# Kernel tuning notes

Hardware: AMD Instinct MI355X
Metric: run time of the kernel (lower is better)

The kernel has to match this reference:

```python
import jax, jax.numpy as jnp
import numpy as np

EMB = 1024
HID = 2048
HEADS = 16
CONV = 4


def causal_conv1d(z, w):
    # z: [B, H, T], w: [H, K] depthwise causal conv
    K = w.shape[1]
    T = z.shape[-1]
    zp = jnp.pad(z, ((0, 0), (0, 0), (K - 1, 0)))  # [B, H, T+K-1]
    out = jnp.zeros_like(z)
    for k in range(K):  # tiny fixed loop over taps (K<=4)
        out = out + w[None, :, k, None] * jax.lax.dynamic_slice_in_dim(zp, k, T, axis=2)
    return out


def linear_scan(a, b):
    # h_t = a_t * h_{t-1} + b_t along last axis; associative scan
    def combine(c1, c2):
        a1, b1 = c1
        a2, b2 = c2
        return a1 * a2, a2 * b1 + b2
    _, h = jax.lax.associative_scan(combine, (a, b), axis=-1)
    return h


def setup_inputs() -> dict:
    key = jax.random.key(0)
    k1, k2, k3, k4 = jax.random.split(key, 4)
    x = jax.random.normal(k1, (4, 2048, EMB), dtype=jnp.float32)
    w1 = jax.random.normal(k2, (3 * HID, EMB), dtype=jnp.float32) * (EMB ** -0.5)
    w2 = jax.random.normal(k3, (EMB, HID), dtype=jnp.float32) * (HID ** -0.5)
    conv_weight = jax.random.normal(k4, (HID, CONV), dtype=jnp.float32) * (CONV ** -0.5)
    return {"x": x, "w1": w1, "w2": w2, "conv_weight": conv_weight}


def reference(x, w1, w2, conv_weight):
    bsz, seq_len, _ = x.shape
    head_dim = HID // HEADS
    y = jnp.einsum("bse,he->bsh", x, w1)  # [B, S, 3*HID]
    out1, z, h = jnp.split(y, 3, axis=-1)
    z = jnp.swapaxes(z, 1, 2)  # [B, HID, S]
    h = jnp.swapaxes(h, 1, 2)
    z = causal_conv1d(z, conv_weight)
    z = jax.nn.sigmoid(z)
    z = z.reshape(bsz * HEADS, head_dim, seq_len)
    h = h.reshape(bsz * HEADS, head_dim, seq_len)
    h = linear_scan(1.0 - z, z * h)
    out2 = jnp.swapaxes(h.reshape(bsz, HID, seq_len), 1, 2)  # [B, S, HID]
    out = jax.nn.silu(out1) * out2
    return jnp.einsum("bsh,eh->bse", out, w2)
```

## Files before the change

### kernel.cpp

```cpp
#include <hip/hip_runtime.h>
#include <cstdint>

#define EMB 1024
#define HID 2048
#define BATCH 4
#define SEQ 2048
#define MROWS (BATCH * SEQ)
#define N1 (3 * HID)
#define K1 EMB
#define N2 EMB
#define K2 HID

#define NX (MROWS * EMB)
#define NW1 (N1 * K1)
#define NW2 (N2 * K2)

#define SEG 32
#define SLEN (SEQ / SEG)

typedef unsigned short ushort_t;
typedef __bf16 bf16x8 __attribute__((ext_vector_type(8)));
typedef float f32x4 __attribute__((ext_vector_type(4)));
typedef ushort_t us4 __attribute__((ext_vector_type(4)));

__device__ __forceinline__ ushort_t f2bf(float f) {
    uint32_t u = __builtin_bit_cast(uint32_t, f);
    u += 0x7fffu + ((u >> 16) & 1u);
    return (ushort_t)(u >> 16);
}
__device__ __forceinline__ float bf2f(ushort_t h) {
    uint32_t u = ((uint32_t)h) << 16;
    return __builtin_bit_cast(float, u);
}
__device__ __forceinline__ float bflo(uint32_t v) {
    return __builtin_bit_cast(float, v << 16);
}
__device__ __forceinline__ float bfhi(uint32_t v) {
    return __builtin_bit_cast(float, v & 0xffff0000u);
}
__device__ __forceinline__ float sigm(float x) {
    return 1.f / (1.f + __expf(-x));
}

__device__ __forceinline__ void gload_lds16(const ushort_t* g, const ushort_t* l) {
    __builtin_amdgcn_global_load_lds(
        (const __attribute__((address_space(1))) void*)(uintptr_t)(g),
        (__attribute__((address_space(3))) void*)(uint32_t)(uintptr_t)(l),
        16, 0, 0);
}

__global__ __launch_bounds__(256) void cvt_kernel(
    const float* __restrict__ x, const float* __restrict__ w1,
    const float* __restrict__ w2, ushort_t* __restrict__ xb,
    ushort_t* __restrict__ w1b, ushort_t* __restrict__ w2b) {
    const int i = (blockIdx.x * 256 + threadIdx.x) * 4;
    const float* s;
    ushort_t* d;
    if (i < NX) {
        s = x + i; d = xb + i;
    } else if (i < NX + NW1) {
        s = w1 + (i - NX); d = w1b + (i - NX);
    } else {
        s = w2 + (i - NX - NW1); d = w2b + (i - NX - NW1);
    }
    const float4 v = *(const float4*)s;
    us4 o;
    o.x = f2bf(v.x); o.y = f2bf(v.y); o.z = f2bf(v.z); o.w = f2bf(v.w);
    *(us4*)d = o;
}

template <bool OUT_BF16>
__global__ __launch_bounds__(256) void gemm_bt(
    const ushort_t* __restrict__ A, const ushort_t* __restrict__ B,
    void* __restrict__ Cv, int M, int N, int K) {
    __shared__ ushort_t sA[2 * 128 * 32];
    __shared__ ushort_t sB[2 * 128 * 32];

    const int tid  = threadIdx.x;
    const int lane = tid & 63;
    const int wave = tid >> 6;
    const int quad = lane >> 4;
    const int l16  = lane & 15;
    const long tm0 = (long)blockIdx.y * 128;
    const long tn0 = (long)blockIdx.x * 128;
    const int wm = (wave & 1) * 64;
    const int wn = (wave >> 1) * 64;

    f32x4 acc[4][4] = {};

    const int ar0 = tid >> 2;
    const int ar1 = (tid + 256) >> 2;
    const int kq  = (tid & 3) ^ ((ar0 >> 1) & 3);
    const int ac  = kq * 8;
    const ushort_t* gA = A + (size_t)tm0 * K;
    const ushort_t* gB = B + (size_t)tn0 * K;

    const int rsw = (l16 >> 1) & 3;
    const int aoff = (quad ^ rsw) * 8 + l16 * 32;

    for (int k0 = 0; k0 < K; k0 += 64) {
        __syncthreads();
#pragma unroll
        for (int p = 0; p < 2; ++p) {
            const int kp = k0 + p * 32;
            ushort_t* pA = &sA[p * 4096];
            ushort_t* pB = &sB[p * 4096];
            gload_lds16(gA + (size_t)ar0 * K + kp + ac, pA + wave * 512);
            gload_lds16(gA + (size_t)ar1 * K + kp + ac, pA + 2048 + wave * 512);
            gload_lds16(gB + (size_t)ar0 * K + kp + ac, pB + wave * 512);
            gload_lds16(gB + (size_t)ar1 * K + kp + ac, pB + 2048 + wave * 512);
        }
        __syncthreads();

#pragma unroll
        for (int p = 0; p < 2; ++p) {
            const ushort_t* pA = &sA[p * 4096];
            const ushort_t* pB = &sB[p * 4096];
            bf16x8 af[4], bfr[4];
#pragma unroll
            for (int i = 0; i < 4; ++i)
                af[i] = *(const bf16x8*)&pA[(wm + i * 16) * 32 + aoff];
#pragma unroll
            for (int j = 0; j < 4; ++j)
                bfr[j] = *(const bf16x8*)&pB[(wn + j * 16) * 32 + aoff];
#pragma unroll
            for (int i = 0; i < 4; ++i)
#pragma unroll
                for (int j = 0; j < 4; ++j)
                    acc[i][j] = __builtin_amdgcn_mfma_f32_16x16x32_bf16(
                        af[i], bfr[j], acc[i][j], 0, 0, 0);
        }
    }

#pragma unroll
    for (int i = 0; i < 4; ++i) {
        const long row0 = tm0 + wm + i * 16 + quad * 4;
#pragma unroll
        for (int j = 0; j < 4; ++j) {
            const long col = tn0 + wn + j * 16 + l16;
#pragma unroll
            for (int r = 0; r < 4; ++r) {
                if constexpr (OUT_BF16) {
                    ((ushort_t*)Cv)[(size_t)(row0 + r) * N + col] = f2bf(acc[i][j][r]);
                } else {
                    ((float*)Cv)[(size_t)(row0 + r) * N + col] = acc[i][j][r];
                }
            }
        }
    }
}

__device__ __forceinline__ void lda4(bf16x8 (&af)[2][4], const ushort_t* c,
                                     int arow, int quad, int sw) {
#pragma unroll
    for (int s = 0; s < 2; ++s)
#pragma unroll
        for (int i = 0; i < 4; ++i)
            af[s][i] = *(const bf16x8*)&c[(arow + i * 16) * 64 +
                                          (((s * 4 + quad) ^ sw) << 3)];
}
__device__ __forceinline__ void ldb2(bf16x8 (&bfr)[2][2], const ushort_t* c,
                                     int bcol, int quad, int sw) {
#pragma unroll
    for (int s = 0; s < 2; ++s)
#pragma unroll
        for (int j = 0; j < 2; ++j)
            bfr[s][j] = *(const bf16x8*)&c[(bcol + j * 16) * 64 +
                                           (((s * 4 + quad) ^ sw) << 3)];
}
template <int QM, int QN>
__device__ __forceinline__ void mm16(f32x4 (&acc)[8][4],
                                     const bf16x8 (&af)[2][4],
                                     const bf16x8 (&bfr)[2][2]) {
#pragma unroll
    for (int s = 0; s < 2; ++s)
#pragma unroll
        for (int i = 0; i < 4; ++i)
#pragma unroll
            for (int j = 0; j < 2; ++j)
                acc[QM * 4 + i][QN * 2 + j] =
                    __builtin_amdgcn_mfma_f32_16x16x32_bf16(
                        af[s][i], bfr[s][j], acc[QM * 4 + i][QN * 2 + j], 0, 0, 0);
}

template <bool OUT_BF16>
__global__ __launch_bounds__(512, 2) void gemm256(
    const ushort_t* __restrict__ A, const ushort_t* __restrict__ B,
    void* __restrict__ Cv, int M, int N, int K) {
    __shared__ __align__(16) ushort_t sA[2][2][8192];
    __shared__ __align__(16) ushort_t sB[2][2][8192];

    const int tid  = threadIdx.x;
    const int lane = tid & 63;
    const int wave = tid >> 6;
    const int wm   = wave >> 2;
    const int wn   = wave & 3;
    const int quad = lane >> 4;
    const int l15  = lane & 15;
    const int sw   = lane & 7;

    int wg = blockIdx.x;
    const int nwg = gridDim.x;
    if ((nwg & 7) == 0) wg = (wg & 7) * (nwg >> 3) + (wg >> 3);
    const int nbx = N >> 8;
    const int bx = wg % nbx;
    const int by = wg / nbx;
    const long tm0 = (long)by << 8;
    const long tn0 = (long)bx << 8;

    const ushort_t* gA = A + (size_t)tm0 * K;
    const ushort_t* gB = B + (size_t)tn0 * K;

    const int l8 = lane >> 3;
    const int ss = (lane & 7) ^ l8;
    const uint32_t rA = (uint32_t)((wave & 3) * 16 + l8 + (wave >> 2) * 128);
    const int cB = wave * 16 + l8;
    const uint32_t rB = (uint32_t)((cB >> 5) * 64 + (cB & 31));
    const uint32_t offA0 = rA * (uint32_t)K + (uint32_t)ss * 8u;
    const uint32_t offA1 = offA0 + 8u * (uint32_t)K;
    const uint32_t offB0 = rB * (uint32_t)K + (uint32_t)ss * 8u;
    const uint32_t offB1 = offB0 + 8u * (uint32_t)K;

    const auto stA = [&](int tt, int q) {
        ushort_t* d = &sA[tt & 1][q][wave << 10];
        const size_t ko = (size_t)tt * 64 + (size_t)q * 64 * (size_t)K;
        gload_lds16(gA + ko + offA0, d);
        gload_lds16(gA + ko + offA1, d + 512);
    };
    const auto stB = [&](int tt, int q) {
        ushort_t* d = &sB[tt & 1][q][wave << 10];
        const size_t ko = (size_t)tt * 64 + (size_t)q * 32 * (size_t)K;
        gload_lds16(gB + ko + offB0, d);
        gload_lds16(gB + ko + offB1, d + 512);
    };

    const int arow = wm * 64 + l15;
    const int bcol = wn * 32 + l15;

    f32x4 acc[8][4] = {};
    bf16x8 af0[2][4], af1[2][4], bf0[2][2], bf1[2][2];

    const int NT = K >> 6;

    stA(0, 0); stB(0, 0); stB(0, 1); stA(0, 1);
    asm volatile("s_waitcnt vmcnt(0)" ::: "memory");
    __builtin_amdgcn_s_barrier();

    for (int T = 0; T < NT; ++T) {
        const int cur = T & 1;
        const ushort_t* a0 = &sA[cur][0][0];
        const ushort_t* a1 = &sA[cur][1][0];
        const ushort_t* b0 = &sB[cur][0][0];
        const ushort_t* b1 = &sB[cur][1][0];
        const bool st1 = (T + 1 < NT);

        lda4(af0, a0, arow, quad, sw);
        ldb2(bf0, b0, bcol, quad, sw);
        ldb2(bf1, b1, bcol, quad, sw);
        lda4(af1, a1, arow, quad, sw);
        if (st1) {
            stA(T + 1, 0); stB(T + 1, 0);
            stB(T + 1, 1); stA(T + 1, 1);
        }
        __builtin_amdgcn_s_setprio(1);
        mm16<0, 0>(acc, af0, bf0);
        mm16<0, 1>(acc, af0, bf1);
        mm16<1, 0>(acc, af1, bf0);
        mm16<1, 1>(acc, af1, bf1);
        __builtin_amdgcn_s_setprio(0);
        if (st1) asm volatile("s_waitcnt vmcnt(0)" ::: "memory");
        __builtin_amdgcn_s_barrier();
    }

#pragma unroll
    for (int ai = 0; ai < 8; ++ai) {
        const long row0 = tm0 + wm * 128 + (ai >> 2) * 64 + (ai & 3) * 16 + quad * 4;
#pragma unroll
        for (int bj = 0; bj < 4; ++bj) {
            const long col = tn0 + wn * 64 + (bj >> 1) * 32 + (bj & 1) * 16 + l15;
#pragma unroll
            for (int r = 0; r < 4; ++r) {
                if constexpr (OUT_BF16) {
                    ((ushort_t*)Cv)[(size_t)(row0 + r) * N + col] = f2bf(acc[ai][bj][r]);
                } else {
                    ((float*)Cv)[(size_t)(row0 + r) * N + col] = acc[ai][bj][r];
                }
            }
        }
    }
}

__global__ __launch_bounds__(256) void scan_part1(
    const ushort_t* __restrict__ y, const float* __restrict__ cw,
    float* __restrict__ Ag, float* __restrict__ Bg) {
    const int gid = blockIdx.x * 256 + threadIdx.x;
    const int ch  = (gid & 1023) * 2;
    const int bs  = gid >> 10;
    const int b   = bs >> 5;
    const int seg = bs & 31;
    const int t0  = seg * SLEN;
    const size_t rowbase = (size_t)b * SEQ;
    const ushort_t* yz = y + 2048 + ch;
    const ushort_t* yh = y + 4096 + ch;

    float w[2][4];
#pragma unroll
    for (int c = 0; c < 2; ++c)
#pragma unroll
        for (int k = 0; k < 4; ++k) w[c][k] = cw[(ch + c) * 4 + k];

    auto ld2 = [&](const ushort_t* p, int t) -> uint32_t {
        return *(const uint32_t*)(p + (rowbase + (size_t)t) * 6144);
    };
    auto zpair = [&](int t, float* out) {
        if (t < 0) { out[0] = 0.f; out[1] = 0.f; }
        else { uint32_t v = ld2(yz, t); out[0] = bflo(v); out[1] = bfhi(v); }
    };

    float z1[2], z2[2], z3[2], A[2] = {1.f, 1.f}, Bv[2] = {0.f, 0.f};
    zpair(t0 - 1, z1); zpair(t0 - 2, z2); zpair(t0 - 3, z3);

#pragma unroll 4
    for (int t = t0; t < t0 + SLEN; ++t) {
        const uint32_t vz = ld2(yz, t);
        const uint32_t vh = ld2(yh, t);
        const float zr[2] = {bflo(vz), bfhi(vz)};
        const float hr[2] = {bflo(vh), bfhi(vh)};
#pragma unroll
        for (int c = 0; c < 2; ++c) {
            const float cv = w[c][0] * z3[c] + w[c][1] * z2[c] +
                             w[c][2] * z1[c] + w[c][3] * zr[c];
            const float s = sigm(cv);
            z3[c] = z2[c]; z2[c] = z1[c]; z1[c] = zr[c];
            const float a = 1.f - s;
            A[c] *= a;
            Bv[c] = a * Bv[c] + s * hr[c];
        }
    }
    const size_t idx = ((size_t)b * SEG + seg) * HID + ch;
    *(float2*)&Ag[idx] = make_float2(A[0], A[1]);
    *(float2*)&Bg[idx] = make_float2(Bv[0], Bv[1]);
}

__global__ __launch_bounds__(256) void scan_part2(
    const float* __restrict__ Ag, const float* __restrict__ Bg,
    float* __restrict__ Cr) {
    const int gid = blockIdx.x * 256 + threadIdx.x;
    const int b  = gid >> 11;
    const int ch = gid & 2047;
    float carry = 0.f;
#pragma unroll
    for (int s = 0; s < SEG; ++s) {
        const size_t idx = ((size_t)b * SEG + s) * HID + ch;
        Cr[idx] = carry;
        carry = Ag[idx] * carry + Bg[idx];
    }
}

__global__ __launch_bounds__(256) void scan_part3(
    const ushort_t* __restrict__ y, const float* __restrict__ cw,
    const float* __restrict__ Cr, ushort_t* __restrict__ u) {
    const int gid = blockIdx.x * 256 + threadIdx.x;
    const int ch  = (gid & 1023) * 2;
    const int bs  = gid >> 10;
    const int b   = bs >> 5;
    const int seg = bs & 31;
    const int t0  = seg * SLEN;
    const size_t rowbase = (size_t)b * SEQ;
    const ushort_t* yo = y + ch;
    const ushort_t* yz = y + 2048 + ch;
    const ushort_t* yh = y + 4096 + ch;

    float w[2][4];
#pragma unroll
    for (int c = 0; c < 2; ++c)
#pragma unroll
        for (int k = 0; k < 4; ++k) w[c][k] = cw[(ch + c) * 4 + k];

    auto ld2 = [&](const ushort_t* p, int t) -> uint32_t {
        return *(const uint32_t*)(p + (rowbase + (size_t)t) * 6144);
    };
    auto zpair = [&](int t, float* out) {
        if (t < 0) { out[0] = 0.f; out[1] = 0.f; }
        else { uint32_t v = ld2(yz, t); out[0] = bflo(v); out[1] = bfhi(v); }
    };

    const size_t cidx = ((size_t)b * SEG + seg) * HID + ch;
    float h[2] = {Cr[cidx], Cr[cidx + 1]};
    float z1[2], z2[2], z3[2];
    zpair(t0 - 1, z1); zpair(t0 - 2, z2); zpair(t0 - 3, z3);

#pragma unroll 4
    for (int t = t0; t < t0 + SLEN; ++t) {
        const uint32_t vz = ld2(yz, t);
        const uint32_t vh = ld2(yh, t);
        const uint32_t vo = ld2(yo, t);
        const float zr[2] = {bflo(vz), bfhi(vz)};
        const float hr[2] = {bflo(vh), bfhi(vh)};
        const float o1[2] = {bflo(vo), bfhi(vo)};
        ushort_t res[2];
#pragma unroll
        for (int c = 0; c < 2; ++c) {
            const float cv = w[c][0] * z3[c] + w[c][1] * z2[c] +
                             w[c][2] * z1[c] + w[c][3] * zr[c];
            const float s = sigm(cv);
            z3[c] = z2[c]; z2[c] = z1[c]; z1[c] = zr[c];
            h[c] = (1.f - s) * h[c] + s * hr[c];
            const float sil = o1[c] * sigm(o1[c]);
            res[c] = f2bf(sil * h[c]);
        }
        *(uint32_t*)&u[(rowbase + (size_t)t) * (size_t)HID + ch] =
            (uint32_t)res[0] | ((uint32_t)res[1] << 16);
    }
}

extern "C" void kernel_launch(void* const* d_in, const int* in_sizes, int n_in,
                              void* d_out, int out_size, void* d_ws, size_t ws_size,
                              hipStream_t stream) {
    const float* x  = (const float*)d_in[0];
    const float* w1 = (const float*)d_in[1];
    const float* w2 = (const float*)d_in[2];
    const float* cw = (const float*)d_in[3];
    char* ws = (char*)d_ws;

    ushort_t* xb  = (ushort_t*)(ws);
    ushort_t* w1b = (ushort_t*)(ws + (size_t)16777216);
    ushort_t* w2b = (ushort_t*)(ws + (size_t)29360128);
    ushort_t* y   = (ushort_t*)(ws + (size_t)33554432);
    ushort_t* u   = (ushort_t*)(ws + (size_t)134217728);
    float* Ag = (float*)(ws);
    float* Bg = (float*)(ws + (size_t)1048576);
    float* Cr = (float*)(ws + (size_t)2097152);
    float* out = (float*)d_out;

    cvt_kernel<<<16384, 256, 0, stream>>>(x, w1, w2, xb, w1b, w2b);
    gemm256<true><<<dim3(768), 512, 0, stream>>>(xb, w1b, (void*)y, MROWS, N1, K1);
    scan_part1<<<512, 256, 0, stream>>>(y, cw, Ag, Bg);
    scan_part2<<<32, 256, 0, stream>>>(Ag, Bg, Cr);
    scan_part3<<<512, 256, 0, stream>>>(y, cw, Cr, u);
    gemm_bt<false><<<dim3(N2 / 128, MROWS / 128), 256, 0, stream>>>(
        u, w2b, (void*)out, MROWS, N2, K2);
}
```

Measured before the change: 306.0 us.

## Split-K second GEMM with atomics and vectorize first GEMM epilogue stores

The second GEMM becomes a split-K kernel with two K halves. Each half accumulates into a zeroed fp32 output through relaxed atomic adds, which doubles the block count from 512 to 1024. Separately, the first GEMM swaps MFMA operands so the accumulator layout is transposed, letting each lane write 4 contiguous outputs as one packed bf16 uint2 store instead of scalar strided stores. Costs are an extra memset of the output and atomic traffic for every output element.

```diff
diff --git a/kernel.cpp b/kernel.cpp
--- a/kernel.cpp
+++ b/kernel.cpp
@@ -69,10 +69,9 @@
     *(us4*)d = o;
 }
 
-template <bool OUT_BF16>
-__global__ __launch_bounds__(256) void gemm_bt(
+__global__ __launch_bounds__(256) void gemm_bt_ks(
     const ushort_t* __restrict__ A, const ushort_t* __restrict__ B,
-    void* __restrict__ Cv, int M, int N, int K) {
+    float* __restrict__ C, int M, int N, int K, int KLEN) {
     __shared__ ushort_t sA[2 * 128 * 32];
     __shared__ ushort_t sB[2 * 128 * 32];
 
@@ -92,13 +91,14 @@
     const int ar1 = (tid + 256) >> 2;
     const int kq  = (tid & 3) ^ ((ar0 >> 1) & 3);
     const int ac  = kq * 8;
-    const ushort_t* gA = A + (size_t)tm0 * K;
-    const ushort_t* gB = B + (size_t)tn0 * K;
+    const size_t kofs = (size_t)blockIdx.z * (size_t)KLEN;
+    const ushort_t* gA = A + (size_t)tm0 * K + kofs;
+    const ushort_t* gB = B + (size_t)tn0 * K + kofs;
 
     const int rsw = (l16 >> 1) & 3;
     const int aoff = (quad ^ rsw) * 8 + l16 * 32;
 
-    for (int k0 = 0; k0 < K; k0 += 64) {
+    for (int k0 = 0; k0 < KLEN; k0 += 64) {
         __syncthreads();
 #pragma unroll
         for (int p = 0; p < 2; ++p) {
@@ -140,11 +140,9 @@
             const long col = tn0 + wn + j * 16 + l16;
 #pragma unroll
             for (int r = 0; r < 4; ++r) {
-                if constexpr (OUT_BF16) {
-                    ((ushort_t*)Cv)[(size_t)(row0 + r) * N + col] = f2bf(acc[i][j][r]);
-                } else {
-                    ((float*)Cv)[(size_t)(row0 + r) * N + col] = acc[i][j][r];
-                }
+                __hip_atomic_fetch_add(&C[(size_t)(row0 + r) * N + col],
+                                       acc[i][j][r], __ATOMIC_RELAXED,
+                                       __HIP_MEMORY_SCOPE_AGENT);
             }
         }
     }
@@ -180,7 +178,7 @@
             for (int j = 0; j < 2; ++j)
                 acc[QM * 4 + i][QN * 2 + j] =
                     __builtin_amdgcn_mfma_f32_16x16x32_bf16(
-                        af[s][i], bfr[s][j], acc[QM * 4 + i][QN * 2 + j], 0, 0, 0);
+                        bfr[s][j], af[s][i], acc[QM * 4 + i][QN * 2 + j], 0, 0, 0);
 }
 
 template <bool OUT_BF16>
@@ -274,17 +272,21 @@
 
 #pragma unroll
     for (int ai = 0; ai < 8; ++ai) {
-        const long row0 = tm0 + wm * 128 + (ai >> 2) * 64 + (ai & 3) * 16 + quad * 4;
+        const long m = tm0 + wm * 128 + (ai >> 2) * 64 + (ai & 3) * 16 + l15;
 #pragma unroll
         for (int bj = 0; bj < 4; ++bj) {
-            const long col = tn0 + wn * 64 + (bj >> 1) * 32 + (bj & 1) * 16 + l15;
-#pragma unroll
-            for (int r = 0; r < 4; ++r) {
-                if constexpr (OUT_BF16) {
-                    ((ushort_t*)Cv)[(size_t)(row0 + r) * N + col] = f2bf(acc[ai][bj][r]);
-                } else {
-                    ((float*)Cv)[(size_t)(row0 + r) * N + col] = acc[ai][bj][r];
-                }
+            const long n0 = tn0 + wn * 64 + (bj >> 1) * 32 + (bj & 1) * 16 + quad * 4;
+            if constexpr (OUT_BF16) {
+                const uint32_t lo = (uint32_t)f2bf(acc[ai][bj][0]) |
+                                    ((uint32_t)f2bf(acc[ai][bj][1]) << 16);
+                const uint32_t hi = (uint32_t)f2bf(acc[ai][bj][2]) |
+                                    ((uint32_t)f2bf(acc[ai][bj][3]) << 16);
+                *(uint2*)&((ushort_t*)Cv)[(size_t)m * N + n0] = make_uint2(lo, hi);
+            } else {
+                float4 v;
+                v.x = acc[ai][bj][0]; v.y = acc[ai][bj][1];
+                v.z = acc[ai][bj][2]; v.w = acc[ai][bj][3];
+                *(float4*)&((float*)Cv)[(size_t)m * N + n0] = v;
             }
         }
     }
@@ -438,6 +440,7 @@
     scan_part1<<<512, 256, 0, stream>>>(y, cw, Ag, Bg);
     scan_part2<<<32, 256, 0, stream>>>(Ag, Bg, Cr);
     scan_part3<<<512, 256, 0, stream>>>(y, cw, Cr, u);
-    gemm_bt<false><<<dim3(N2 / 128, MROWS / 128), 256, 0, stream>>>(
-        u, w2b, (void*)out, MROWS, N2, K2);
-}
+    hipMemsetAsync(d_out, 0, (size_t)MROWS * N2 * 4, stream);
+    gemm_bt_ks<<<dim3(N2 / 128, MROWS / 128, 2), 256, 0, stream>>>(
+        u, w2b, out, MROWS, N2, K2, K2 / 2);
+}
```

Result: slower. 357.5 us (+16.8%).

## Replace second GEMM with double-buffered 256x128 tile kernel

Applied to the files above, without the earlier changes.

Swaps the simple 128x128 gemm_bt used for the output projection for a new gemm_mn kernel. It uses 512 threads, 256x128 tiles, a double-buffered LDS pipeline that prefetches the next K-tile while MFMAs run, s_setprio around the MFMA block, and an XCD-aware remapping of workgroup IDs. The intent is to hide global-load latency and improve data reuse per block. In exchange it uses more LDS per block and launches only 256 workgroups, which may reduce occupancy and balance across CUs.

```diff
diff --git a/kernel.cpp b/kernel.cpp
--- a/kernel.cpp
+++ b/kernel.cpp
@@ -67,87 +67,6 @@
     us4 o;
     o.x = f2bf(v.x); o.y = f2bf(v.y); o.z = f2bf(v.z); o.w = f2bf(v.w);
     *(us4*)d = o;
-}
-
-template <bool OUT_BF16>
-__global__ __launch_bounds__(256) void gemm_bt(
-    const ushort_t* __restrict__ A, const ushort_t* __restrict__ B,
-    void* __restrict__ Cv, int M, int N, int K) {
-    __shared__ ushort_t sA[2 * 128 * 32];
-    __shared__ ushort_t sB[2 * 128 * 32];
-
-    const int tid  = threadIdx.x;
-    const int lane = tid & 63;
-    const int wave = tid >> 6;
-    const int quad = lane >> 4;
-    const int l16  = lane & 15;
-    const long tm0 = (long)blockIdx.y * 128;
-    const long tn0 = (long)blockIdx.x * 128;
-    const int wm = (wave & 1) * 64;
-    const int wn = (wave >> 1) * 64;
-
-    f32x4 acc[4][4] = {};
-
-    const int ar0 = tid >> 2;
-    const int ar1 = (tid + 256) >> 2;
-    const int kq  = (tid & 3) ^ ((ar0 >> 1) & 3);
-    const int ac  = kq * 8;
-    const ushort_t* gA = A + (size_t)tm0 * K;
-    const ushort_t* gB = B + (size_t)tn0 * K;
-
-    const int rsw = (l16 >> 1) & 3;
-    const int aoff = (quad ^ rsw) * 8 + l16 * 32;
-
-    for (int k0 = 0; k0 < K; k0 += 64) {
-        __syncthreads();
-#pragma unroll
-        for (int p = 0; p < 2; ++p) {
-            const int kp = k0 + p * 32;
-            ushort_t* pA = &sA[p * 4096];
-            ushort_t* pB = &sB[p * 4096];
-            gload_lds16(gA + (size_t)ar0 * K + kp + ac, pA + wave * 512);
-            gload_lds16(gA + (size_t)ar1 * K + kp + ac, pA + 2048 + wave * 512);
-            gload_lds16(gB + (size_t)ar0 * K + kp + ac, pB + wave * 512);
-            gload_lds16(gB + (size_t)ar1 * K + kp + ac, pB + 2048 + wave * 512);
-        }
-        __syncthreads();
-
-#pragma unroll
-        for (int p = 0; p < 2; ++p) {
-            const ushort_t* pA = &sA[p * 4096];
-            const ushort_t* pB = &sB[p * 4096];
-            bf16x8 af[4], bfr[4];
-#pragma unroll
-            for (int i = 0; i < 4; ++i)
-                af[i] = *(const bf16x8*)&pA[(wm + i * 16) * 32 + aoff];
-#pragma unroll
-            for (int j = 0; j < 4; ++j)
-                bfr[j] = *(const bf16x8*)&pB[(wn + j * 16) * 32 + aoff];
-#pragma unroll
-            for (int i = 0; i < 4; ++i)
-#pragma unroll
-                for (int j = 0; j < 4; ++j)
-                    acc[i][j] = __builtin_amdgcn_mfma_f32_16x16x32_bf16(
-                        af[i], bfr[j], acc[i][j], 0, 0, 0);
-        }
-    }
-
-#pragma unroll
-    for (int i = 0; i < 4; ++i) {
-        const long row0 = tm0 + wm + i * 16 + quad * 4;
-#pragma unroll
-        for (int j = 0; j < 4; ++j) {
-            const long col = tn0 + wn + j * 16 + l16;
-#pragma unroll
-            for (int r = 0; r < 4; ++r) {
-                if constexpr (OUT_BF16) {
-                    ((ushort_t*)Cv)[(size_t)(row0 + r) * N + col] = f2bf(acc[i][j][r]);
-                } else {
-                    ((float*)Cv)[(size_t)(row0 + r) * N + col] = acc[i][j][r];
-                }
-            }
-        }
-    }
 }
 
 __device__ __forceinline__ void lda4(bf16x8 (&af)[2][4], const ushort_t* c,
@@ -290,6 +209,104 @@
     }
 }
 
+__global__ __launch_bounds__(512, 2) void gemm_mn(
+    const ushort_t* __restrict__ A, const ushort_t* __restrict__ B,
+    float* __restrict__ C, int M, int N, int K) {
+    __shared__ __align__(16) ushort_t sA[2][2][8192];
+    __shared__ __align__(16) ushort_t sB[2][8192];
+
+    const int tid  = threadIdx.x;
+    const int lane = tid & 63;
+    const int wave = tid >> 6;
+    const int wm   = wave >> 1;
+    const int wn   = wave & 1;
+    const int quad = lane >> 4;
+    const int l15  = lane & 15;
+    const int sw   = lane & 7;
+
+    int wg = blockIdx.x;
+    const int nwg = gridDim.x;
+    if ((nwg & 7) == 0) wg = (wg & 7) * (nwg >> 3) + (wg >> 3);
+    const int nbx = N >> 7;
+    const int bx = wg % nbx;
+    const int by = wg / nbx;
+    const long tm0 = (long)by << 8;
+    const long tn0 = (long)bx << 7;
+
+    const ushort_t* gA = A + (size_t)tm0 * K;
+    const ushort_t* gB = B + (size_t)tn0 * K;
+
+    const int l8 = lane >> 3;
+    const int ss = (lane & 7) ^ l8;
+    const uint32_t rA = (uint32_t)((wave & 3) * 16 + l8 + (wave >> 2) * 128);
+    const uint32_t rB = (uint32_t)(wave * 16 + l8);
+    const uint32_t offA0 = rA * (uint32_t)K + (uint32_t)ss * 8u;
+    const uint32_t offA1 = offA0 + 8u * (uint32_t)K;
+    const uint32_t offB0 = rB * (uint32_t)K + (uint32_t)ss * 8u;
+    const uint32_t offB1 = offB0 + 8u * (uint32_t)K;
+
+    const auto stA = [&](int tt, int q) {
+        ushort_t* d = &sA[tt & 1][q][wave << 10];
+        const size_t ko = (size_t)tt * 64 + (size_t)q * 64 * (size_t)K;
+        gload_lds16(gA + ko + offA0, d);
+        gload_lds16(gA + ko + offA1, d + 512);
+    };
+    const auto stB = [&](int tt) {
+        ushort_t* d = &sB[tt & 1][wave << 10];
+        const size_t ko = (size_t)tt * 64;
+        gload_lds16(gB + ko + offB0, d);
+        gload_lds16(gB + ko + offB1, d + 512);
+    };
+
+    const int cq   = wm & 1;
+    const int arow = (wm >> 1) * 64 + l15;
+    const int bcol = wn * 64 + l15;
+
+    f32x4 acc[4][4] = {};
+    bf16x8 af[2][4], bf[2][4];
+
+    const int NT = K >> 6;
+
+    stA(0, 0); stA(0, 1); stB(0);
+    asm volatile("s_waitcnt vmcnt(0)" ::: "memory");
+    __builtin_amdgcn_s_barrier();
+
+    for (int T = 0; T < NT; ++T) {
+        const int cur = T & 1;
+        const ushort_t* pa = &sA[cur][cq][0];
+        const ushort_t* pb = &sB[cur][0];
+        const bool st1 = (T + 1 < NT);
+
+        lda4(af, pa, arow, quad, sw);
+        lda4(bf, pb, bcol, quad, sw);
+        if (st1) { stA(T + 1, 0); stA(T + 1, 1); stB(T + 1); }
+        __builtin_amdgcn_s_setprio(1);
+#pragma unroll
+        for (int s = 0; s < 2; ++s)
+#pragma unroll
+            for (int i = 0; i < 4; ++i)
+#pragma unroll
+                for (int j = 0; j < 4; ++j)
+                    acc[i][j] = __builtin_amdgcn_mfma_f32_16x16x32_bf16(
+                        af[s][i], bf[s][j], acc[i][j], 0, 0, 0);
+        __builtin_amdgcn_s_setprio(0);
+        if (st1) asm volatile("s_waitcnt vmcnt(0)" ::: "memory");
+        __builtin_amdgcn_s_barrier();
+    }
+
+#pragma unroll
+    for (int i = 0; i < 4; ++i) {
+        const long row0 = tm0 + wm * 64 + i * 16 + quad * 4;
+#pragma unroll
+        for (int j = 0; j < 4; ++j) {
+            const long col = tn0 + wn * 64 + j * 16 + l15;
+#pragma unroll
+            for (int r = 0; r < 4; ++r)
+                C[(size_t)(row0 + r) * N + col] = acc[i][j][r];
+        }
+    }
+}
+
 __global__ __launch_bounds__(256) void scan_part1(
     const ushort_t* __restrict__ y, const float* __restrict__ cw,
     float* __restrict__ Ag, float* __restrict__ Bg) {
@@ -438,6 +455,5 @@
     scan_part1<<<512, 256, 0, stream>>>(y, cw, Ag, Bg);
     scan_part2<<<32, 256, 0, stream>>>(Ag, Bg, Cr);
     scan_part3<<<512, 256, 0, stream>>>(y, cw, Cr, u);
-    gemm_bt<false><<<dim3(N2 / 128, MROWS / 128), 256, 0, stream>>>(
-        u, w2b, (void*)out, MROWS, N2, K2);
-}
+    gemm_mn<<<dim3(256), 512, 0, stream>>>(u, w2b, out, MROWS, N2, K2);
+}
```

Result: faster. 298.9 us (-2.3%).
